# Optimization experiments

Hardware: AMD Instinct MI355X
Metric: run time of the kernel (lower is better)

Reference implementation:

```python
import jax, jax.numpy as jnp
import numpy as np

V0 = 25; WIN = 3; NS = 6; EPS = 1e-5

def _build_scales():
    # ring graph on 25 joints (matches A_binary in init_kwargs)
    A = np.zeros((V0, V0), np.float32)
    for i in range(V0):
        A[i, (i + 1) % V0] = 1.0; A[(i + 1) % V0, i] = 1.0
    AL = np.tile(A + np.eye(V0, dtype=A.dtype), (WIN, WIN))  # spatial-temporal graph (75x75)
    I = np.eye(len(AL), dtype=AL.dtype)
    def shell(k):
        return np.minimum(np.linalg.matrix_power(AL + I, k), 1) - np.minimum(np.linalg.matrix_power(AL + I, k - 1), 1)
    def kadj(k):
        return I.copy() if k == 0 else shell(k) + I  # with_self=True
    def norm(g):
        dinv = np.power(g.sum(-1), -0.5)
        Dm = np.eye(len(g)) * dinv
        return (Dm @ g @ Dm).astype(np.float32)
    def klap(k):
        if k == 0:
            return I.astype(np.float32)
        Ak = shell(k)
        D = Ak.sum(-1)
        Dm = np.eye(len(D)) * np.power(D, -0.5)
        return (Dm @ (np.eye(len(D)) * (D + 2) - Ak) @ Dm).astype(np.float32)
    A_scales = np.concatenate([norm(kadj(k)) for k in range(NS)])  # (NS*75, 75)
    B_scales = np.concatenate([klap(k) for k in range(NS)])        # (NS*75, 75)
    return jnp.asarray(A_scales), jnp.asarray(B_scales)

def _bn(x, g, b):
    # BatchNorm2d in training mode: batch stats over (N, T, V)
    m = x.mean(axis=(0, 2, 3), keepdims=True)
    v = x.var(axis=(0, 2, 3), keepdims=True)
    return (x - m) * jax.lax.rsqrt(v + EPS) * g[None, :, None, None] + b[None, :, None, None]

def setup_inputs():
    key = jax.random.key(0)
    ks = jax.random.split(key, 4)
    N, C, T = 8, 96, 128
    A_scales, B_scales = _build_scales()
    d_in = C * NS * 2
    return {
        'x': jax.random.normal(ks[0], (N, C, T, V0), jnp.float32),
        'A_scales': A_scales,
        'B_scales': B_scales,
        'A_res': jax.random.uniform(ks[1], A_scales.shape, jnp.float32, -1e-6, 1e-6),
        'W_mlp': jax.random.normal(ks[2], (C, d_in), jnp.float32) / np.sqrt(d_in),
        'b_mlp': jnp.zeros((C,), jnp.float32),
        'g1': jnp.ones((C,), jnp.float32),
        'bt1': jnp.zeros((C,), jnp.float32),
        'W_out': jax.random.normal(ks[3], (C, C, WIN), jnp.float32) / np.sqrt(C * WIN),
        'b_out': jnp.zeros((C,), jnp.float32),
        'g2': jnp.ones((C,), jnp.float32),
        'bt2': jnp.zeros((C,), jnp.float32),
    }

def _forward(x, A_scales, B_scales, A_res, W_mlp, b_mlp, g1, bt1, W_out, b_out, g2, bt2):
    N, C, T, V = x.shape
    xp = jnp.pad(x, ((0, 0), (0, 0), (1, 1), (0, 0)))
    xu = jnp.stack([xp[:, :, w:w + T, :] for w in range(WIN)], axis=3).reshape(N, C, T, WIN * V)
    VL = WIN * V
    A = A_scales + A_res
    B = B_scales + A_res
    def agg(M):
        a = jnp.einsum('vu,nctu->nctv', M, xu)               # (N, C, T, NS*VL)
        a = a.reshape(N, C, T, NS, VL).transpose(0, 3, 1, 2, 4)
        return a.reshape(N, NS * C, T, VL)
    h = jnp.concatenate([agg(A), agg(B)], axis=1)            # (N, 2*NS*C, T, VL)
    # MLP: 1x1 conv -> ReLU -> BN
    h = jnp.einsum('oi,nitv->notv', W_mlp, h) + b_mlp[None, :, None, None]
    h = _bn(jax.nn.relu(h), g1, bt1)
    h = jax.nn.relu(h)                                       # gcn: act(mlp + residual(=0))
    h = h.reshape(N, C, T, WIN, V)
    out = jnp.einsum('oiw,nitwv->notv', W_out, h) + b_out[None, :, None, None]
    return _bn(out, g2, bt2)

def reference(x, A_scales, B_scales, A_res, W_mlp, b_mlp, g1, bt1, W_out, b_out, g2, bt2):
    return _forward(x, A_scales, B_scales, A_res, W_mlp, b_mlp, g1, bt1, W_out, b_out, g2, bt2)
```

## Files before the change

### kernel.cpp

```cpp
#include <hip/hip_runtime.h>


#define NB 8
#define CB 96
#define TB 128
#define VB 25
#define VLB 75
#define EPSB 1e-5f
#define XRS 104
#define T2S 104
#define HBS 296

typedef __attribute__((ext_vector_type(8))) short bf16x8;
typedef __attribute__((ext_vector_type(4))) short short4v;
typedef __attribute__((ext_vector_type(4))) float f32x4;
typedef __attribute__((ext_vector_type(2))) unsigned int uint2v;
typedef __attribute__((ext_vector_type(4))) unsigned int uint4v;

__device__ inline unsigned short f2bf(float f) {
  unsigned int u = __float_as_uint(f);
  u = (u + 0x7FFFu + ((u >> 16) & 1u)) >> 16;
  return (unsigned short)u;
}
__device__ inline float bf2f(unsigned short u) {
  return __uint_as_float(((unsigned int)u) << 16);
}
__device__ inline unsigned pack2bf(float lo, float hi) {
  return (unsigned)f2bf(lo) | ((unsigned)f2bf(hi) << 16);
}

__global__ __launch_bounds__(256) void k0_init(
    const float* __restrict__ As, const float* __restrict__ Bs,
    const float* __restrict__ Ar, const float* __restrict__ Wm,
    const float* __restrict__ Wo,
    unsigned short* __restrict__ ABsw, unsigned short* __restrict__ Wsw,
    unsigned short* __restrict__ Wosw, float* __restrict__ stats) {
  int i = blockIdx.x * 256 + threadIdx.x;
  if (i < 110592) {
    int ps = i / 9216, r = i % 9216;
    int wv = r / 1536, r2 = r % 1536;
    int kk = r2 / 512, r3 = r2 % 512;
    int lane = r3 / 8, j = r3 % 8;
    int o = wv * 16 + (lane & 15);
    int c = kk * 32 + (lane >> 4) * 8 + j;
    Wsw[i] = f2bf(Wm[o * 1152 + ps * 96 + c]);
  }
  if (i < 92160) {
    int ps = i / 7680, r = i % 7680;
    int nt = r / 1536, r2 = r % 1536;
    int kk = r2 / 512, r3 = r2 % 512;
    int lane = r3 / 8, j = r3 % 8;
    int u = nt * 16 + (lane & 15);
    int up = kk * 32 + (lane >> 4) * 8 + j;
    float v = 0.f;
    if (u < 75 && up < 75) {
      int path = ps / 6, s = ps % 6;
      int idx = (s * 75 + u) * 75 + up;
      v = (path == 0 ? As[idx] : Bs[idx]) + Ar[idx];
    }
    ABsw[i] = f2bf(v);
  }
  if (i < 27648) {
    int wv = i / 4608, r = i % 4608;
    int kk = r / 512, r3 = r % 512;
    int lane = r3 / 8, j = r3 % 8;
    int o = wv * 16 + (lane & 15);
    int k = kk * 32 + (lane >> 4) * 8 + j;
    Wosw[i] = f2bf(Wo[o * 288 + k]);
  }
  if (i < 384) stats[i] = 0.f;
}

__global__ __launch_bounds__(384, 2) void k1t2(
    const float* __restrict__ x, const unsigned short* __restrict__ ABsw,
    const unsigned short* __restrict__ Wsw, const float* __restrict__ bm,
    unsigned short* __restrict__ h_relu, float* __restrict__ stats1) {
  __shared__ unsigned short xraw[112 * XRS];
  __shared__ unsigned short tmp2[6][2][16 * T2S];
  __shared__ float st1s[96], st2s[96];
  const int tid = threadIdx.x;
  const int n = blockIdx.x >> 6, t0 = (blockIdx.x & 63) * 2;
  const int wave = tid >> 6, lane = tid & 63;
  const int l15 = lane & 15, quad = lane >> 4, q8 = quad * 8;
  const int wrow16 = wave * 16;

  for (int idx = tid; idx < 96 * 112; idx += 384) {
    int c = idx / 112, r = idx - c * 112;
    float v = 0.f;
    if (r < 100) {
      int tt = t0 - 1 + r / 25, vv = r % 25;
      if (tt >= 0 && tt < TB) v = x[((n * CB + c) * TB + tt) * VB + vv];
    }
    xraw[r * XRS + c] = f2bf(v);
  }
  for (int idx = tid; idx < 6 * 2 * 256; idx += 384) {
    int w = idx >> 9, rm = idx & 511;
    int d = rm >> 8, e = rm & 255;
    tmp2[w][d][(e >> 4) * T2S + 80 + (e & 15)] = 0;
  }
  __syncthreads();

  const f32x4 zf = {0.f, 0.f, 0.f, 0.f};
  f32x4 acc2[2][5];
#pragma unroll
  for (int d = 0; d < 2; ++d)
#pragma unroll
    for (int nt = 0; nt < 5; ++nt) acc2[d][nt] = zf;

  const unsigned short* Wbase = Wsw + wave * 1536 + lane * 8;
  const unsigned short* Bbase = ABsw + lane * 8;
  unsigned short* tw0 = &tmp2[wave][0][l15 * T2S + quad * 4];
  unsigned short* tw1 = &tmp2[wave][1][l15 * T2S + quad * 4];
  const unsigned short* tr0 = &tmp2[wave][0][l15 * T2S + q8];
  const unsigned short* tr1 = &tmp2[wave][1][l15 * T2S + q8];

#pragma unroll
  for (int ps = 0; ps < 12; ++ps) {
    bf16x8 wa[3];
#pragma unroll
    for (int kk = 0; kk < 3; ++kk)
      wa[kk] = *reinterpret_cast<const bf16x8*>(Wbase + ps * 9216 + kk * 512);
    bf16x8 bf[15];
#pragma unroll
    for (int i = 0; i < 15; ++i)
      bf[i] = *reinterpret_cast<const bf16x8*>(Bbase + ps * 7680 + i * 512);

    f32x4 acc1[5];
#pragma unroll
    for (int nt = 0; nt < 5; ++nt) acc1[nt] = zf;
#pragma unroll
    for (int kk = 0; kk < 3; ++kk)
#pragma unroll
      for (int nt = 0; nt < 5; ++nt) {
        bf16x8 a = *reinterpret_cast<const bf16x8*>(&xraw[(nt * 16 + l15) * XRS + kk * 32 + q8]);
        acc1[nt] = __builtin_amdgcn_mfma_f32_16x16x32_bf16(a, wa[kk], acc1[nt], 0, 0, 0);
      }
#pragma unroll
    for (int nt = 0; nt < 5; ++nt) {
      unsigned p01 = pack2bf(acc1[nt][0], acc1[nt][1]);
      unsigned p23 = pack2bf(acc1[nt][2], acc1[nt][3]);
      *reinterpret_cast<short4v*>(tw0 + nt * 16) =
          __builtin_bit_cast(short4v, (uint2v){p01, p23});
    }
#pragma unroll
    for (int nt = 0; nt < 5; ++nt) acc1[nt] = zf;
#pragma unroll
    for (int kk = 0; kk < 3; ++kk)
#pragma unroll
      for (int nt = 0; nt < 5; ++nt) {
        bf16x8 a = *reinterpret_cast<const bf16x8*>(&xraw[(25 + nt * 16 + l15) * XRS + kk * 32 + q8]);
        acc1[nt] = __builtin_amdgcn_mfma_f32_16x16x32_bf16(a, wa[kk], acc1[nt], 0, 0, 0);
      }
#pragma unroll
    for (int nt = 0; nt < 5; ++nt) {
      unsigned p01 = pack2bf(acc1[nt][0], acc1[nt][1]);
      unsigned p23 = pack2bf(acc1[nt][2], acc1[nt][3]);
      *reinterpret_cast<short4v*>(tw1 + nt * 16) =
          __builtin_bit_cast(short4v, (uint2v){p01, p23});
    }

    asm volatile("" ::: "memory");
    __builtin_amdgcn_sched_barrier(0);

#pragma unroll
    for (int kk = 0; kk < 3; ++kk) {
      bf16x8 a0 = *reinterpret_cast<const bf16x8*>(tr0 + kk * 32);
#pragma unroll
      for (int nt = 0; nt < 5; ++nt)
        acc2[0][nt] = __builtin_amdgcn_mfma_f32_16x16x32_bf16(a0, bf[nt * 3 + kk], acc2[0][nt], 0, 0, 0);
      bf16x8 a1 = *reinterpret_cast<const bf16x8*>(tr1 + kk * 32);
#pragma unroll
      for (int nt = 0; nt < 5; ++nt)
        acc2[1][nt] = __builtin_amdgcn_mfma_f32_16x16x32_bf16(a1, bf[nt * 3 + kk], acc2[1][nt], 0, 0, 0);
    }

    asm volatile("" ::: "memory");
    __builtin_amdgcn_sched_barrier(0);
  }

  const int orow = wrow16 + quad * 4;
  float s1[4] = {0.f, 0.f, 0.f, 0.f}, s2[4] = {0.f, 0.f, 0.f, 0.f};
  unsigned short* hp = h_relu + (unsigned)(n * TB + t0) * 7200;
#pragma unroll
  for (int d = 0; d < 2; ++d) {
#pragma unroll
    for (int r = 0; r < 4; ++r) {
      const int o = orow + r;
      const float bias = bm[o];
#pragma unroll
      for (int nt = 0; nt < 5; ++nt) {
        int u = nt * 16 + l15;
        if (u < VLB) {
          float v = acc2[d][nt][r] + bias;
          v = v > 0.f ? v : 0.f;
          int w = u / 25, vv = u - w * 25;
          hp[d * 7200 + vv * 288 + o * 3 + w] = f2bf(v);
          s1[r] += v;
          s2[r] += v * v;
        }
      }
    }
  }
#pragma unroll
  for (int off = 1; off < 16; off <<= 1) {
#pragma unroll
    for (int r = 0; r < 4; ++r) {
      s1[r] += __shfl_xor(s1[r], off, 64);
      s2[r] += __shfl_xor(s2[r], off, 64);
    }
  }
  if (l15 == 0) {
#pragma unroll
    for (int r = 0; r < 4; ++r) { st1s[orow + r] = s1[r]; st2s[orow + r] = s2[r]; }
  }
  __syncthreads();
  if (tid < 96) {
    atomicAdd(&stats1[tid], st1s[tid]);
    atomicAdd(&stats1[96 + tid], st2s[tid]);
  }
}

__global__ __launch_bounds__(384) void k3n(
    const unsigned short* __restrict__ h_relu, const float* __restrict__ stats1,
    const float* __restrict__ g1, const float* __restrict__ bt1,
    const unsigned short* __restrict__ Wosw, const float* __restrict__ bo,
    float* __restrict__ out_pre) {
  __shared__ unsigned short hnb[2][32 * HBS];
  __shared__ float a1s[96], b1s[96];
  const int tid = threadIdx.x;
  const int n = blockIdx.x >> 6, t0 = (blockIdx.x & 63) * 2;

  if (tid < 96) {
    const float inv = 1.f / (8.f * 128.f * 75.f);
    float m = stats1[tid] * inv;
    float var = stats1[96 + tid] * inv - m * m;
    float a = g1[tid] * rsqrtf(var + EPSB);
    a1s[tid] = a;
    b1s[tid] = bt1[tid] - m * a;
  }
  for (int idx = tid; idx < 2 * 7 * HBS; idx += 384) {
    int d = idx / (7 * HBS), rm = idx % (7 * HBS);
    hnb[d][25 * HBS + rm] = 0;
  }
  __syncthreads();

  const unsigned short* hp = h_relu + (unsigned)(n * TB + t0) * 7200;
  for (int i8 = tid; i8 < 1800; i8 += 384) {
    bf16x8 v = *reinterpret_cast<const bf16x8*>(hp + i8 * 8);
    int e = i8 * 8;
    int d = e / 7200;
    int er = e - d * 7200;
    int vv = er / 288, c = er - vv * 288;
    float f[8];
#pragma unroll
    for (int j = 0; j < 8; ++j) {
      int ic = (c + j) / 3;
      float val = a1s[ic] * bf2f((unsigned short)v[j]) + b1s[ic];
      f[j] = val > 0.f ? val : 0.f;
    }
    unsigned dw0 = pack2bf(f[0], f[1]);
    unsigned dw1 = pack2bf(f[2], f[3]);
    unsigned dw2 = pack2bf(f[4], f[5]);
    unsigned dw3 = pack2bf(f[6], f[7]);
    *reinterpret_cast<uint4v*>(&hnb[d][vv * HBS + c]) = (uint4v){dw0, dw1, dw2, dw3};
  }
  __syncthreads();

  const int wave = tid >> 6, lane = tid & 63;
  const int l15 = lane & 15, quad = lane >> 4, q8 = quad * 8;
  const f32x4 zf = {0.f, 0.f, 0.f, 0.f};
  f32x4 acc[2][2] = {{zf, zf}, {zf, zf}};
  const unsigned short* Apw = Wosw + wave * 4608 + lane * 8;
#pragma unroll
  for (int kk = 0; kk < 9; ++kk) {
    bf16x8 a = *reinterpret_cast<const bf16x8*>(Apw + kk * 512);
#pragma unroll
    for (int d = 0; d < 2; ++d) {
      bf16x8 b0 = *reinterpret_cast<const bf16x8*>(&hnb[d][l15 * HBS + kk * 32 + q8]);
      bf16x8 b1 = *reinterpret_cast<const bf16x8*>(&hnb[d][(16 + l15) * HBS + kk * 32 + q8]);
      acc[d][0] = __builtin_amdgcn_mfma_f32_16x16x32_bf16(a, b0, acc[d][0], 0, 0, 0);
      acc[d][1] = __builtin_amdgcn_mfma_f32_16x16x32_bf16(a, b1, acc[d][1], 0, 0, 0);
    }
  }

  const int orow = wave * 16 + quad * 4;
#pragma unroll
  for (int d = 0; d < 2; ++d) {
#pragma unroll
    for (int nt = 0; nt < 2; ++nt) {
      int v = nt * 16 + l15;
      if (v < VB) {
#pragma unroll
        for (int r = 0; r < 4; ++r) {
          const int o = orow + r;
          out_pre[((n * CB + o) * TB + t0 + d) * VB + v] = acc[d][nt][r] + bo[o];
        }
      }
    }
  }
}

__global__ __launch_bounds__(256) void k4_stats(
    const float* __restrict__ out_pre, float* __restrict__ stats2) {
  __shared__ float ws1[4], ws2[4];
  const int tid = threadIdx.x;
  const int o = blockIdx.x % CB, p = blockIdx.x / CB;
  float s1 = 0.f, s2 = 0.f;
#pragma unroll
  for (int k = 0; k < 2; ++k) {
    const int n = 2 * p + k;
    const f32x4* base = reinterpret_cast<const f32x4*>(out_pre + (n * CB + o) * (TB * VB));
    for (int idx = tid; idx < TB * VB / 4; idx += 256) {
      f32x4 v = base[idx];
#pragma unroll
      for (int j = 0; j < 4; ++j) { s1 += v[j]; s2 += v[j] * v[j]; }
    }
  }
#pragma unroll
  for (int off = 1; off < 64; off <<= 1) {
    s1 += __shfl_xor(s1, off, 64);
    s2 += __shfl_xor(s2, off, 64);
  }
  const int wave = tid >> 6;
  if ((tid & 63) == 0) { ws1[wave] = s1; ws2[wave] = s2; }
  __syncthreads();
  if (tid == 0) {
    float r1 = ws1[0] + ws1[1] + ws1[2] + ws1[3];
    float r2 = ws2[0] + ws2[1] + ws2[2] + ws2[3];
    atomicAdd(&stats2[o], r1);
    atomicAdd(&stats2[96 + o], r2);
  }
}

__global__ __launch_bounds__(256) void k5_bn2(
    const float* __restrict__ out_pre, const float* __restrict__ stats2,
    const float* __restrict__ g2, const float* __restrict__ bt2,
    float* __restrict__ out) {
  int idx = blockIdx.x * 256 + threadIdx.x;
  if (idx >= NB * CB * TB * VB / 4) return;
  int o = (idx / (TB * VB / 4)) % CB;
  const float inv = 1.f / (8.f * 128.f * 25.f);
  float m = stats2[o] * inv;
  float var = stats2[96 + o] * inv - m * m;
  float a = g2[o] * rsqrtf(var + EPSB);
  float b = bt2[o] - m * a;
  f32x4 vin = reinterpret_cast<const f32x4*>(out_pre)[idx];
  f32x4 vo;
#pragma unroll
  for (int j = 0; j < 4; ++j) vo[j] = a * vin[j] + b;
  reinterpret_cast<f32x4*>(out)[idx] = vo;
}

extern "C" void kernel_launch(void* const* d_in, const int* in_sizes, int n_in,
                              void* d_out, int out_size, void* d_ws, size_t ws_size,
                              hipStream_t stream) {
  const float* x   = (const float*)d_in[0];
  const float* As  = (const float*)d_in[1];
  const float* Bs  = (const float*)d_in[2];
  const float* Ar  = (const float*)d_in[3];
  const float* Wm  = (const float*)d_in[4];
  const float* bm  = (const float*)d_in[5];
  const float* g1  = (const float*)d_in[6];
  const float* bt1 = (const float*)d_in[7];
  const float* Wo  = (const float*)d_in[8];
  const float* bo  = (const float*)d_in[9];
  const float* g2  = (const float*)d_in[10];
  const float* bt2 = (const float*)d_in[11];
  float* out = (float*)d_out;

  char* base = (char*)d_ws;
  unsigned short* HR   = (unsigned short*)base;
  float* out_pre       = (float*)(base + 14745600);
  unsigned short* ABsw = (unsigned short*)(base + 24576000);
  unsigned short* Wsw  = (unsigned short*)(base + 24760320);
  unsigned short* Wosw = (unsigned short*)(base + 24981504);
  float* stats         = (float*)(base + 25036800);
  float* stats1 = stats, *stats2 = stats + 192;

  k0_init<<<432, 256, 0, stream>>>(As, Bs, Ar, Wm, Wo, ABsw, Wsw, Wosw, stats);
  k1t2<<<NB * TB / 2, 384, 0, stream>>>(x, ABsw, Wsw, bm, HR, stats1);
  k3n<<<NB * TB / 2, 384, 0, stream>>>(HR, stats1, g1, bt1, Wosw, bo, out_pre);
  k4_stats<<<CB * 4, 256, 0, stream>>>(out_pre, stats2);
  k5_bn2<<<(NB * CB * TB * VB / 4 + 255) / 256, 256, 0, stream>>>(out_pre, stats2, g2, bt2, out);
}
```

Before: 180.3 us.

## Double-buffer graph-matrix fragments in LDS via async global_load_lds prefetch

The per-scale B-operand fragments used to be loaded straight from global memory into registers inside each scale iteration. They are now prefetched one scale ahead into a double-buffered LDS region with global_load_lds, with a block barrier at the top of each iteration. The two per-wave temp tiles are merged into one reused buffer, and the two second-stage MFMA passes are interleaved so the LDS freed by the merge can hold the staging buffers. The change aims to hide global latency and share the loads across waves, at the cost of a block-wide barrier every iteration and more LDS pressure, which may lower occupancy.

```diff
diff --git a/kernel.cpp b/kernel.cpp
--- a/kernel.cpp
+++ b/kernel.cpp
@@ -16,6 +16,9 @@
 typedef __attribute__((ext_vector_type(4))) float f32x4;
 typedef __attribute__((ext_vector_type(2))) unsigned int uint2v;
 typedef __attribute__((ext_vector_type(4))) unsigned int uint4v;
+
+typedef __attribute__((address_space(1))) const unsigned int guint;
+typedef __attribute__((address_space(3))) unsigned int luint;
 
 __device__ inline unsigned short f2bf(float f) {
   unsigned int u = __float_as_uint(f);
@@ -76,7 +79,8 @@
     const unsigned short* __restrict__ Wsw, const float* __restrict__ bm,
     unsigned short* __restrict__ h_relu, float* __restrict__ stats1) {
   __shared__ unsigned short xraw[112 * XRS];
-  __shared__ unsigned short tmp2[6][2][16 * T2S];
+  __shared__ unsigned short tmp2[6][16 * T2S];
+  __shared__ unsigned short absbuf[2][7680];
   __shared__ float st1s[96], st2s[96];
   const int tid = threadIdx.x;
   const int n = blockIdx.x >> 6, t0 = (blockIdx.x & 63) * 2;
@@ -93,12 +97,16 @@
     }
     xraw[r * XRS + c] = f2bf(v);
   }
-  for (int idx = tid; idx < 6 * 2 * 256; idx += 384) {
-    int w = idx >> 9, rm = idx & 511;
-    int d = rm >> 8, e = rm & 255;
-    tmp2[w][d][(e >> 4) * T2S + 80 + (e & 15)] = 0;
-  }
-  __syncthreads();
+  for (int idx = tid; idx < 6 * 16 * 16; idx += 384) {
+    int w = idx >> 8, e = idx & 255;
+    tmp2[w][(e >> 4) * T2S + 80 + (e & 15)] = 0;
+  }
+  {
+    const unsigned short* gsrc = ABsw;
+    for (int c = wave; c < 15; c += 6)
+      __builtin_amdgcn_global_load_lds((guint*)(const void*)(gsrc + c * 512 + lane * 8),
+                                       (luint*)(void*)(&absbuf[0][c * 512]), 16, 0, 0);
+  }
 
   const f32x4 zf = {0.f, 0.f, 0.f, 0.f};
   f32x4 acc2[2][5];
@@ -108,22 +116,29 @@
     for (int nt = 0; nt < 5; ++nt) acc2[d][nt] = zf;
 
   const unsigned short* Wbase = Wsw + wave * 1536 + lane * 8;
-  const unsigned short* Bbase = ABsw + lane * 8;
-  unsigned short* tw0 = &tmp2[wave][0][l15 * T2S + quad * 4];
-  unsigned short* tw1 = &tmp2[wave][1][l15 * T2S + quad * 4];
-  const unsigned short* tr0 = &tmp2[wave][0][l15 * T2S + q8];
-  const unsigned short* tr1 = &tmp2[wave][1][l15 * T2S + q8];
+  unsigned short* tw = &tmp2[wave][l15 * T2S + quad * 4];
+  const unsigned short* tr = &tmp2[wave][l15 * T2S + q8];
 
 #pragma unroll
   for (int ps = 0; ps < 12; ++ps) {
+    __syncthreads();
+    if (ps < 11) {
+      const unsigned short* gsrc = ABsw + (ps + 1) * 7680;
+      unsigned short* lb = absbuf[(ps + 1) & 1];
+      for (int c = wave; c < 15; c += 6)
+        __builtin_amdgcn_global_load_lds((guint*)(const void*)(gsrc + c * 512 + lane * 8),
+                                         (luint*)(void*)(lb + c * 512), 16, 0, 0);
+    }
+
     bf16x8 wa[3];
 #pragma unroll
     for (int kk = 0; kk < 3; ++kk)
       wa[kk] = *reinterpret_cast<const bf16x8*>(Wbase + ps * 9216 + kk * 512);
+    const unsigned short* bb = absbuf[ps & 1] + lane * 8;
     bf16x8 bf[15];
 #pragma unroll
     for (int i = 0; i < 15; ++i)
-      bf[i] = *reinterpret_cast<const bf16x8*>(Bbase + ps * 7680 + i * 512);
+      bf[i] = *reinterpret_cast<const bf16x8*>(bb + i * 512);
 
     f32x4 acc1[5];
 #pragma unroll
@@ -139,9 +154,21 @@
     for (int nt = 0; nt < 5; ++nt) {
       unsigned p01 = pack2bf(acc1[nt][0], acc1[nt][1]);
       unsigned p23 = pack2bf(acc1[nt][2], acc1[nt][3]);
-      *reinterpret_cast<short4v*>(tw0 + nt * 16) =
+      *reinterpret_cast<short4v*>(tw + nt * 16) =
           __builtin_bit_cast(short4v, (uint2v){p01, p23});
     }
+    asm volatile("" ::: "memory");
+    __builtin_amdgcn_sched_barrier(0);
+#pragma unroll
+    for (int kk = 0; kk < 3; ++kk) {
+      bf16x8 a0 = *reinterpret_cast<const bf16x8*>(tr + kk * 32);
+#pragma unroll
+      for (int nt = 0; nt < 5; ++nt)
+        acc2[0][nt] = __builtin_amdgcn_mfma_f32_16x16x32_bf16(a0, bf[nt * 3 + kk], acc2[0][nt], 0, 0, 0);
+    }
+    asm volatile("" ::: "memory");
+    __builtin_amdgcn_sched_barrier(0);
+
 #pragma unroll
     for (int nt = 0; nt < 5; ++nt) acc1[nt] = zf;
 #pragma unroll
@@ -155,25 +182,18 @@
     for (int nt = 0; nt < 5; ++nt) {
       unsigned p01 = pack2bf(acc1[nt][0], acc1[nt][1]);
       unsigned p23 = pack2bf(acc1[nt][2], acc1[nt][3]);
-      *reinterpret_cast<short4v*>(tw1 + nt * 16) =
+      *reinterpret_cast<short4v*>(tw + nt * 16) =
           __builtin_bit_cast(short4v, (uint2v){p01, p23});
     }
-
     asm volatile("" ::: "memory");
     __builtin_amdgcn_sched_barrier(0);
-
 #pragma unroll
     for (int kk = 0; kk < 3; ++kk) {
-      bf16x8 a0 = *reinterpret_cast<const bf16x8*>(tr0 + kk * 32);
-#pragma unroll
-      for (int nt = 0; nt < 5; ++nt)
-        acc2[0][nt] = __builtin_amdgcn_mfma_f32_16x16x32_bf16(a0, bf[nt * 3 + kk], acc2[0][nt], 0, 0, 0);
-      bf16x8 a1 = *reinterpret_cast<const bf16x8*>(tr1 + kk * 32);
+      bf16x8 a1 = *reinterpret_cast<const bf16x8*>(tr + kk * 32);
 #pragma unroll
       for (int nt = 0; nt < 5; ++nt)
         acc2[1][nt] = __builtin_amdgcn_mfma_f32_16x16x32_bf16(a1, bf[nt * 3 + kk], acc2[1][nt], 0, 0, 0);
     }
-
     asm volatile("" ::: "memory");
     __builtin_amdgcn_sched_barrier(0);
   }
```

After: 192.5 us. 6.8% more time.

## Split k1t2 work across 12 waves, one per output-channel group and time step

Applied to the files above, without the earlier changes.

The fused aggregation+MLP kernel now launches 768 threads per block instead of 384. Each wave handles one 16-channel output group for a single time step rather than both time steps. This halves per-wave accumulator state and serial MFMA chains, which should raise occupancy and latency hiding. In exchange, each pair of waves loads the same weight and graph fragments from global memory separately, and the launch bound asks for 6 blocks per CU, which constrains registers more tightly.

```diff
diff --git a/kernel.cpp b/kernel.cpp
--- a/kernel.cpp
+++ b/kernel.cpp
@@ -71,20 +71,20 @@
   if (i < 384) stats[i] = 0.f;
 }
 
-__global__ __launch_bounds__(384, 2) void k1t2(
+__global__ __launch_bounds__(768, 6) void k1t2(
     const float* __restrict__ x, const unsigned short* __restrict__ ABsw,
     const unsigned short* __restrict__ Wsw, const float* __restrict__ bm,
     unsigned short* __restrict__ h_relu, float* __restrict__ stats1) {
   __shared__ unsigned short xraw[112 * XRS];
-  __shared__ unsigned short tmp2[6][2][16 * T2S];
-  __shared__ float st1s[96], st2s[96];
+  __shared__ unsigned short tmp2[12][16 * T2S];
+  __shared__ float st1s[2][96], st2s[2][96];
   const int tid = threadIdx.x;
   const int n = blockIdx.x >> 6, t0 = (blockIdx.x & 63) * 2;
   const int wave = tid >> 6, lane = tid & 63;
+  const int wo = wave >> 1, dt = wave & 1;
   const int l15 = lane & 15, quad = lane >> 4, q8 = quad * 8;
-  const int wrow16 = wave * 16;
-
-  for (int idx = tid; idx < 96 * 112; idx += 384) {
+
+  for (int idx = tid; idx < 96 * 112; idx += 768) {
     int c = idx / 112, r = idx - c * 112;
     float v = 0.f;
     if (r < 100) {
@@ -93,26 +93,22 @@
     }
     xraw[r * XRS + c] = f2bf(v);
   }
-  for (int idx = tid; idx < 6 * 2 * 256; idx += 384) {
-    int w = idx >> 9, rm = idx & 511;
-    int d = rm >> 8, e = rm & 255;
-    tmp2[w][d][(e >> 4) * T2S + 80 + (e & 15)] = 0;
+  for (int idx = tid; idx < 12 * 256; idx += 768) {
+    int w = idx >> 8, e = idx & 255;
+    tmp2[w][(e >> 4) * T2S + 80 + (e & 15)] = 0;
   }
   __syncthreads();
 
   const f32x4 zf = {0.f, 0.f, 0.f, 0.f};
-  f32x4 acc2[2][5];
-#pragma unroll
-  for (int d = 0; d < 2; ++d)
-#pragma unroll
-    for (int nt = 0; nt < 5; ++nt) acc2[d][nt] = zf;
-
-  const unsigned short* Wbase = Wsw + wave * 1536 + lane * 8;
+  f32x4 acc2[5];
+#pragma unroll
+  for (int nt = 0; nt < 5; ++nt) acc2[nt] = zf;
+
+  const unsigned short* Wbase = Wsw + wo * 1536 + lane * 8;
   const unsigned short* Bbase = ABsw + lane * 8;
-  unsigned short* tw0 = &tmp2[wave][0][l15 * T2S + quad * 4];
-  unsigned short* tw1 = &tmp2[wave][1][l15 * T2S + quad * 4];
-  const unsigned short* tr0 = &tmp2[wave][0][l15 * T2S + q8];
-  const unsigned short* tr1 = &tmp2[wave][1][l15 * T2S + q8];
+  unsigned short* tw = &tmp2[wave][l15 * T2S + quad * 4];
+  const unsigned short* tr = &tmp2[wave][l15 * T2S + q8];
+  const int xoff = dt * 25;
 
 #pragma unroll
   for (int ps = 0; ps < 12; ++ps) {
@@ -132,72 +128,47 @@
     for (int kk = 0; kk < 3; ++kk)
 #pragma unroll
       for (int nt = 0; nt < 5; ++nt) {
-        bf16x8 a = *reinterpret_cast<const bf16x8*>(&xraw[(nt * 16 + l15) * XRS + kk * 32 + q8]);
+        bf16x8 a = *reinterpret_cast<const bf16x8*>(&xraw[(xoff + nt * 16 + l15) * XRS + kk * 32 + q8]);
         acc1[nt] = __builtin_amdgcn_mfma_f32_16x16x32_bf16(a, wa[kk], acc1[nt], 0, 0, 0);
       }
 #pragma unroll
     for (int nt = 0; nt < 5; ++nt) {
       unsigned p01 = pack2bf(acc1[nt][0], acc1[nt][1]);
       unsigned p23 = pack2bf(acc1[nt][2], acc1[nt][3]);
-      *reinterpret_cast<short4v*>(tw0 + nt * 16) =
+      *reinterpret_cast<short4v*>(tw + nt * 16) =
           __builtin_bit_cast(short4v, (uint2v){p01, p23});
     }
-#pragma unroll
-    for (int nt = 0; nt < 5; ++nt) acc1[nt] = zf;
-#pragma unroll
-    for (int kk = 0; kk < 3; ++kk)
-#pragma unroll
-      for (int nt = 0; nt < 5; ++nt) {
-        bf16x8 a = *reinterpret_cast<const bf16x8*>(&xraw[(25 + nt * 16 + l15) * XRS + kk * 32 + q8]);
-        acc1[nt] = __builtin_amdgcn_mfma_f32_16x16x32_bf16(a, wa[kk], acc1[nt], 0, 0, 0);
-      }
-#pragma unroll
-    for (int nt = 0; nt < 5; ++nt) {
-      unsigned p01 = pack2bf(acc1[nt][0], acc1[nt][1]);
-      unsigned p23 = pack2bf(acc1[nt][2], acc1[nt][3]);
-      *reinterpret_cast<short4v*>(tw1 + nt * 16) =
-          __builtin_bit_cast(short4v, (uint2v){p01, p23});
-    }
-
     asm volatile("" ::: "memory");
     __builtin_amdgcn_sched_barrier(0);
 
 #pragma unroll
     for (int kk = 0; kk < 3; ++kk) {
-      bf16x8 a0 = *reinterpret_cast<const bf16x8*>(tr0 + kk * 32);
+      bf16x8 a0 = *reinterpret_cast<const bf16x8*>(tr + kk * 32);
 #pragma unroll
       for (int nt = 0; nt < 5; ++nt)
-        acc2[0][nt] = __builtin_amdgcn_mfma_f32_16x16x32_bf16(a0, bf[nt * 3 + kk], acc2[0][nt], 0, 0, 0);
-      bf16x8 a1 = *reinterpret_cast<const bf16x8*>(tr1 + kk * 32);
-#pragma unroll
-      for (int nt = 0; nt < 5; ++nt)
-        acc2[1][nt] = __builtin_amdgcn_mfma_f32_16x16x32_bf16(a1, bf[nt * 3 + kk], acc2[1][nt], 0, 0, 0);
-    }
-
+        acc2[nt] = __builtin_amdgcn_mfma_f32_16x16x32_bf16(a0, bf[nt * 3 + kk], acc2[nt], 0, 0, 0);
+    }
     asm volatile("" ::: "memory");
     __builtin_amdgcn_sched_barrier(0);
   }
 
-  const int orow = wrow16 + quad * 4;
+  const int orow = wo * 16 + quad * 4;
   float s1[4] = {0.f, 0.f, 0.f, 0.f}, s2[4] = {0.f, 0.f, 0.f, 0.f};
-  unsigned short* hp = h_relu + (unsigned)(n * TB + t0) * 7200;
-#pragma unroll
-  for (int d = 0; d < 2; ++d) {
-#pragma unroll
-    for (int r = 0; r < 4; ++r) {
-      const int o = orow + r;
-      const float bias = bm[o];
-#pragma unroll
-      for (int nt = 0; nt < 5; ++nt) {
-        int u = nt * 16 + l15;
-        if (u < VLB) {
-          float v = acc2[d][nt][r] + bias;
-          v = v > 0.f ? v : 0.f;
-          int w = u / 25, vv = u - w * 25;
-          hp[d * 7200 + vv * 288 + o * 3 + w] = f2bf(v);
-          s1[r] += v;
-          s2[r] += v * v;
-        }
+  unsigned short* hp = h_relu + (unsigned)(n * TB + t0) * 7200 + dt * 7200;
+#pragma unroll
+  for (int r = 0; r < 4; ++r) {
+    const int o = orow + r;
+    const float bias = bm[o];
+#pragma unroll
+    for (int nt = 0; nt < 5; ++nt) {
+      int u = nt * 16 + l15;
+      if (u < VLB) {
+        float v = acc2[nt][r] + bias;
+        v = v > 0.f ? v : 0.f;
+        int w = u / 25, vv = u - w * 25;
+        hp[vv * 288 + o * 3 + w] = f2bf(v);
+        s1[r] += v;
+        s2[r] += v * v;
       }
     }
   }
@@ -211,12 +182,12 @@
   }
   if (l15 == 0) {
 #pragma unroll
-    for (int r = 0; r < 4; ++r) { st1s[orow + r] = s1[r]; st2s[orow + r] = s2[r]; }
+    for (int r = 0; r < 4; ++r) { st1s[dt][orow + r] = s1[r]; st2s[dt][orow + r] = s2[r]; }
   }
   __syncthreads();
   if (tid < 96) {
-    atomicAdd(&stats1[tid], st1s[tid]);
-    atomicAdd(&stats1[96 + tid], st2s[tid]);
+    atomicAdd(&stats1[tid], st1s[0][tid] + st1s[1][tid]);
+    atomicAdd(&stats1[96 + tid], st2s[0][tid] + st2s[1][tid]);
   }
 }
 
@@ -378,7 +349,7 @@
   float* stats1 = stats, *stats2 = stats + 192;
 
   k0_init<<<432, 256, 0, stream>>>(As, Bs, Ar, Wm, Wo, ABsw, Wsw, Wosw, stats);
-  k1t2<<<NB * TB / 2, 384, 0, stream>>>(x, ABsw, Wsw, bm, HR, stats1);
+  k1t2<<<NB * TB / 2, 768, 0, stream>>>(x, ABsw, Wsw, bm, HR, stats1);
   k3n<<<NB * TB / 2, 384, 0, stream>>>(HR, stats1, g1, bt1, Wosw, bo, out_pre);
   k4_stats<<<CB * 4, 256, 0, stream>>>(out_pre, stats2);
   k5_bn2<<<(NB * CB * TB * VB / 4 + 255) / 256, 256, 0, stream>>>(out_pre, stats2, g2, bt2, out);
```

New measurement: 269.0 us. +49.2%, slower.
